# Kernel optimization log

Measured on AMD Instinct MI355X. Metric: run time of the kernel, lower is better.

## Reference

```python
import jax, jax.numpy as jnp
import numpy as np

B, C, N, T = 16, 32, 1024, 128
R = 10  # low-rank bottleneck of W1/W2


def setup_inputs() -> dict:
    key = jax.random.key(0)
    k1, k2, k3, k4 = jax.random.split(key, 4)
    x = jax.random.normal(k1, (B, C, N, T), dtype=jnp.float32)
    W1 = jax.random.normal(k2, (R, N), dtype=jnp.float32) * 0.05
    W2 = jax.random.normal(k3, (R, N), dtype=jnp.float32) * 0.05
    alpha = jax.random.normal(k4, (C,), dtype=jnp.float32) * 0.1
    return {"x": x, "W1": W1, "W2": W2, "alpha": alpha}


def reference(x, W1, W2, alpha):
    # k = q = einsum('bint,i->btn', x, alpha): contract channels -> [B, T, N]
    k = jnp.einsum('bcnt,c->btn', x, alpha)
    # low-rank bilinear scores: (k @ W1^T) @ (k @ W2^T)^T -> [B, T, T]
    kw1 = jnp.einsum('btn,rn->btr', k, W1)   # [B, T, R]
    qw2 = jnp.einsum('btn,rn->btr', k, W2)   # [B, T, R]
    scores = jnp.einsum('btr,bsr->bts', kw1, qw2)  # [B, T, T]
    att = jax.nn.softmax(scores, axis=-1)
    # weighted sum over time: einsum('bti,bcni->bcnt', att, x)
    return jnp.einsum('bts,bcns->bcnt', att, x)
```

## Files before the change

kernel.cpp:

```cpp
#include <hip/hip_runtime.h>
#include <hip/hip_bf16.h>


#define B_ 16
#define C_ 32
#define N_ 1024
#define T_ 128
#define R_ 10

typedef __bf16 bf16x8 __attribute__((ext_vector_type(8)));
typedef __bf16 bf16x4 __attribute__((ext_vector_type(4)));
typedef float f32x4 __attribute__((ext_vector_type(4)));

__global__ __launch_bounds__(256) void k_reduce_c(const float* __restrict__ x,
                                                  const float* __restrict__ alpha,
                                                  float* __restrict__ k) {
    int bid = blockIdx.x;
    int b   = bid >> 7;
    int nc  = bid & 127;
    int tid = threadIdx.x;
    int nl  = tid >> 5;
    int lc  = tid & 31;
    int n   = nc * 8 + nl;
    const float4* xb = reinterpret_cast<const float4*>(
        x + ((size_t)(b * C_) * N_ + n) * T_) + lc;
    float4 acc = {0.f, 0.f, 0.f, 0.f};
    #pragma unroll 8
    for (int c = 0; c < C_; ++c) {
        float a = alpha[c];
        float4 v = xb[(size_t)c * (N_ * T_ / 4)];
        acc.x += a * v.x; acc.y += a * v.y; acc.z += a * v.z; acc.w += a * v.w;
    }
    reinterpret_cast<float4*>(k + ((size_t)b * N_ + n) * T_)[lc] = acc;
}

__global__ __launch_bounds__(128) void kw_partial2(const float* __restrict__ k,
                                                   const float* __restrict__ W1,
                                                   const float* __restrict__ W2,
                                                   float* __restrict__ p1,
                                                   float* __restrict__ p2) {
    __shared__ float wl[32][20];
    int bid = blockIdx.x;
    int b   = bid >> 5;
    int ch  = bid & 31;
    int n0  = ch * 32;
    int t   = threadIdx.x;
    for (int i = t; i < 32 * 20; i += 128) {
        int nl = i & 31, q = i >> 5;
        wl[nl][q] = (q < 10) ? W1[q * N_ + n0 + nl] : W2[(q - 10) * N_ + n0 + nl];
    }
    __syncthreads();
    float a1[R_] = {}, a2[R_] = {};
    const float* kb = k + ((size_t)b * N_ + n0) * T_ + t;
    #pragma unroll 2
    for (int g = 0; g < 4; ++g) {
        float kv[8];
        #pragma unroll
        for (int j = 0; j < 8; ++j) kv[j] = kb[(g * 8 + j) * T_];
        #pragma unroll
        for (int j = 0; j < 8; ++j) {
            int nl = g * 8 + j;
            #pragma unroll
            for (int r = 0; r < R_; ++r) {
                a1[r] += kv[j] * wl[nl][r];
                a2[r] += kv[j] * wl[nl][10 + r];
            }
        }
    }
    #pragma unroll
    for (int r = 0; r < R_; ++r) {
        size_t o = (((size_t)b * R_ + r) * 32 + ch) * T_ + t;
        p1[o] = a1[r];
        p2[o] = a2[r];
    }
}

__global__ __launch_bounds__(128) void kw_reduce(const float* __restrict__ p1,
                                                 const float* __restrict__ p2,
                                                 float* __restrict__ kwc) {
    int bid = blockIdx.x;
    int b = bid / 20;
    int q = bid - b * 20;
    int w = q / 10;
    int r = q - w * 10;
    int t = threadIdx.x;
    const float* src = (w ? p2 : p1) + (((size_t)b * R_ + r) * 32) * T_ + t;
    float s = 0.f;
    #pragma unroll
    for (int ch = 0; ch < 32; ++ch) s += src[ch * T_];
    kwc[(((size_t)b * 2 + w) * R_ + r) * T_ + t] = s;
}

__global__ __launch_bounds__(128) void scores_softmax(const float* __restrict__ kwc,
                                                      __bf16* __restrict__ att) {
    __shared__ __align__(16) float kw1s[T_][12];
    __shared__ __align__(16) float kw2s[T_][12];
    __shared__ float sc[T_][T_ + 1];
    int b = blockIdx.x;
    int t = threadIdx.x;
    const float* kb = kwc + (size_t)b * 2 * R_ * T_;
    #pragma unroll
    for (int r = 0; r < R_; ++r) {
        kw1s[t][r] = kb[r * T_ + t];
        kw2s[t][r] = kb[(R_ + r) * T_ + t];
    }
    __syncthreads();
    float myw[R_];
    #pragma unroll
    for (int r = 0; r < R_; ++r) myw[r] = kw1s[t][r];
    float mx = -1e30f;
    for (int s = 0; s < T_; ++s) {
        float wv[12];
        const float4* qr = reinterpret_cast<const float4*>(&kw2s[s][0]);
        #pragma unroll
        for (int q = 0; q < 3; ++q) *reinterpret_cast<float4*>(&wv[q * 4]) = qr[q];
        float v = 0.f;
        #pragma unroll
        for (int r = 0; r < R_; ++r) v += myw[r] * wv[r];
        sc[t][s] = v;
        mx = fmaxf(mx, v);
    }
    float sum = 0.f;
    for (int s = 0; s < T_; ++s) {
        float e = __expf(sc[t][s] - mx);
        sc[t][s] = e;
        sum += e;
    }
    float inv = 1.0f / sum;
    __bf16* arow = att + ((size_t)b * T_ + t) * T_;
    for (int s8 = 0; s8 < T_; s8 += 8) {
        bf16x8 hv;
        #pragma unroll
        for (int q = 0; q < 8; ++q) hv[q] = (__bf16)(sc[t][s8 + q] * inv);
        *reinterpret_cast<bf16x8*>(arow + s8) = hv;
    }
}

__global__ __launch_bounds__(256, 4) void out_gemm2(const float* __restrict__ x,
                                                    const __bf16* __restrict__ att,
                                                    float* __restrict__ out) {
    __shared__ __align__(16) __bf16 attl[T_][T_];
    int bid = blockIdx.x;
    int nc  = bid & 15;
    int c   = (bid >> 4) & 31;
    int b   = bid >> 9;
    int tid = threadIdx.x;
    size_t slab = ((size_t)(b * C_ + c) * N_ + nc * 64) * T_;
    char* attb = (char*)&attl[0][0];

    const uint4* ga = reinterpret_cast<const uint4*>(att + (size_t)b * T_ * T_);
    #pragma unroll
    for (int i = 0; i < 8; ++i) {
        int e = i * 256 + tid, row = e >> 4;
        int bc = ((e & 15) * 16) ^ ((row & 7) << 4);
        *reinterpret_cast<uint4*>(attb + row * 256 + bc) = ga[e];
    }
    __syncthreads();

    int wave = tid >> 6, lane = tid & 63;
    int r16 = lane & 15, g = lane >> 4;
    int wt = wave & 1, wn = wave >> 1;
    int swz = (r16 & 7) << 4;

    const float* xr0 = x + slab + (size_t)(wn * 32 + r16) * T_ + g * 8;
    const float* xr1 = xr0 + 16 * T_;

    f32x4 acc[2][4] = {};
    float4 c0a = *reinterpret_cast<const float4*>(xr0);
    float4 c0b = *reinterpret_cast<const float4*>(xr0 + 4);
    float4 c1a = *reinterpret_cast<const float4*>(xr1);
    float4 c1b = *reinterpret_cast<const float4*>(xr1 + 4);
    #pragma unroll
    for (int ks = 0; ks < 4; ++ks) {
        float4 n0a, n0b, n1a, n1b;
        if (ks < 3) {
            int o = (ks + 1) * 32;
            n0a = *reinterpret_cast<const float4*>(xr0 + o);
            n0b = *reinterpret_cast<const float4*>(xr0 + o + 4);
            n1a = *reinterpret_cast<const float4*>(xr1 + o);
            n1b = *reinterpret_cast<const float4*>(xr1 + o + 4);
        }
        bf16x8 bx0 = {(__bf16)c0a.x, (__bf16)c0a.y, (__bf16)c0a.z, (__bf16)c0a.w,
                      (__bf16)c0b.x, (__bf16)c0b.y, (__bf16)c0b.z, (__bf16)c0b.w};
        bf16x8 bx1 = {(__bf16)c1a.x, (__bf16)c1a.y, (__bf16)c1a.z, (__bf16)c1a.w,
                      (__bf16)c1b.x, (__bf16)c1b.y, (__bf16)c1b.z, (__bf16)c1b.w};
        int kc = ks * 64 + g * 16;
        bf16x8 a[4];
        #pragma unroll
        for (int tt = 0; tt < 4; ++tt)
            a[tt] = *reinterpret_cast<const bf16x8*>(
                attb + (wt * 64 + tt * 16 + r16) * 256 + (kc ^ swz));
        #pragma unroll
        for (int tt = 0; tt < 4; ++tt)
            acc[0][tt] = __builtin_amdgcn_mfma_f32_16x16x32_bf16(a[tt], bx0, acc[0][tt], 0, 0, 0);
        #pragma unroll
        for (int tt = 0; tt < 4; ++tt)
            acc[1][tt] = __builtin_amdgcn_mfma_f32_16x16x32_bf16(a[tt], bx1, acc[1][tt], 0, 0, 0);
        c0a = n0a; c0b = n0b; c1a = n1a; c1b = n1b;
    }
    float* o = out + slab;
    #pragma unroll
    for (int nn = 0; nn < 2; ++nn) {
        int n_l = wn * 32 + nn * 16 + r16;
        #pragma unroll
        for (int tt = 0; tt < 4; ++tt)
            *reinterpret_cast<f32x4*>(o + (size_t)n_l * T_ + (wt * 64 + tt * 16 + g * 4)) = acc[nn][tt];
    }
}

extern "C" void kernel_launch(void* const* d_in, const int* in_sizes, int n_in,
                              void* d_out, int out_size, void* d_ws, size_t ws_size,
                              hipStream_t stream) {
    const float* x     = (const float*)d_in[0];
    const float* W1    = (const float*)d_in[1];
    const float* W2    = (const float*)d_in[2];
    const float* alpha = (const float*)d_in[3];
    float* out = (float*)d_out;

    float* k    = (float*)d_ws;
    float* p1   = k   + (size_t)B_ * N_ * T_;
    float* p2   = p1  + (size_t)B_ * R_ * 32 * T_;
    float* kwc  = p2  + (size_t)B_ * R_ * 32 * T_;
    __bf16* att = (__bf16*)(kwc + (size_t)B_ * 2 * R_ * T_);

    k_reduce_c   <<<dim3(B_ * (N_ / 8)), dim3(256), 0, stream>>>(x, alpha, k);
    kw_partial2  <<<dim3(B_ * 32),       dim3(128), 0, stream>>>(k, W1, W2, p1, p2);
    kw_reduce    <<<dim3(B_ * 20),       dim3(128), 0, stream>>>(p1, p2, kwc);
    scores_softmax<<<dim3(B_),           dim3(128), 0, stream>>>(kwc, att);
    out_gemm2    <<<dim3(B_ * 512),      dim3(256), 0, stream>>>(x, att, out);
}
```

Measured before the change: 214.3 us.

## Stage x tiles in LDS and loop four n-chunks per block, reusing att

```diff
diff --git a/kernel.cpp b/kernel.cpp
--- a/kernel.cpp
+++ b/kernel.cpp
@@ -136,24 +136,39 @@
     }
 }
 
-__global__ __launch_bounds__(256, 4) void out_gemm2(const float* __restrict__ x,
+__global__ __launch_bounds__(256, 3) void out_gemm3(const float* __restrict__ x,
                                                     const __bf16* __restrict__ att,
                                                     float* __restrict__ out) {
     __shared__ __align__(16) __bf16 attl[T_][T_];
-    int bid = blockIdx.x;
-    int nc  = bid & 15;
-    int c   = (bid >> 4) & 31;
-    int b   = bid >> 9;
+    __shared__ __align__(16) __bf16 xsl[64][T_];
+    int bid = blockIdx.x;
+    int sg  = bid & 3;
+    int c   = (bid >> 2) & 31;
+    int b   = bid >> 7;
     int tid = threadIdx.x;
-    size_t slab = ((size_t)(b * C_ + c) * N_ + nc * 64) * T_;
     char* attb = (char*)&attl[0][0];
+    char* xbb  = (char*)&xsl[0][0];
+    size_t slab0 = ((size_t)(b * C_ + c) * N_ + (sg * 4) * 64) * T_;
 
     const uint4* ga = reinterpret_cast<const uint4*>(att + (size_t)b * T_ * T_);
+    uint4 ar[8];
+    #pragma unroll
+    for (int i = 0; i < 8; ++i) ar[i] = ga[i * 256 + tid];
+    const float4* gx0 = reinterpret_cast<const float4*>(x + slab0);
+    float4 xr[8];
+    #pragma unroll
+    for (int j = 0; j < 8; ++j) xr[j] = gx0[j * 256 + tid];
     #pragma unroll
     for (int i = 0; i < 8; ++i) {
         int e = i * 256 + tid, row = e >> 4;
         int bc = ((e & 15) * 16) ^ ((row & 7) << 4);
-        *reinterpret_cast<uint4*>(attb + row * 256 + bc) = ga[e];
+        *reinterpret_cast<uint4*>(attb + row * 256 + bc) = ar[i];
+    }
+    #pragma unroll
+    for (int j = 0; j < 8; ++j) {
+        int e = j * 256 + tid, row = e >> 5;
+        bf16x4 hv = {(__bf16)xr[j].x, (__bf16)xr[j].y, (__bf16)xr[j].z, (__bf16)xr[j].w};
+        *reinterpret_cast<bf16x4*>(xbb + row * 256 + (((e & 31) * 8) ^ ((row & 7) << 4))) = hv;
     }
     __syncthreads();
 
@@ -162,49 +177,55 @@
     int wt = wave & 1, wn = wave >> 1;
     int swz = (r16 & 7) << 4;
 
-    const float* xr0 = x + slab + (size_t)(wn * 32 + r16) * T_ + g * 8;
-    const float* xr1 = xr0 + 16 * T_;
-
-    f32x4 acc[2][4] = {};
-    float4 c0a = *reinterpret_cast<const float4*>(xr0);
-    float4 c0b = *reinterpret_cast<const float4*>(xr0 + 4);
-    float4 c1a = *reinterpret_cast<const float4*>(xr1);
-    float4 c1b = *reinterpret_cast<const float4*>(xr1 + 4);
-    #pragma unroll
-    for (int ks = 0; ks < 4; ++ks) {
-        float4 n0a, n0b, n1a, n1b;
-        if (ks < 3) {
-            int o = (ks + 1) * 32;
-            n0a = *reinterpret_cast<const float4*>(xr0 + o);
-            n0b = *reinterpret_cast<const float4*>(xr0 + o + 4);
-            n1a = *reinterpret_cast<const float4*>(xr1 + o);
-            n1b = *reinterpret_cast<const float4*>(xr1 + o + 4);
-        }
-        bf16x8 bx0 = {(__bf16)c0a.x, (__bf16)c0a.y, (__bf16)c0a.z, (__bf16)c0a.w,
-                      (__bf16)c0b.x, (__bf16)c0b.y, (__bf16)c0b.z, (__bf16)c0b.w};
-        bf16x8 bx1 = {(__bf16)c1a.x, (__bf16)c1a.y, (__bf16)c1a.z, (__bf16)c1a.w,
-                      (__bf16)c1b.x, (__bf16)c1b.y, (__bf16)c1b.z, (__bf16)c1b.w};
-        int kc = ks * 64 + g * 16;
-        bf16x8 a[4];
-        #pragma unroll
-        for (int tt = 0; tt < 4; ++tt)
-            a[tt] = *reinterpret_cast<const bf16x8*>(
-                attb + (wt * 64 + tt * 16 + r16) * 256 + (kc ^ swz));
-        #pragma unroll
-        for (int tt = 0; tt < 4; ++tt)
-            acc[0][tt] = __builtin_amdgcn_mfma_f32_16x16x32_bf16(a[tt], bx0, acc[0][tt], 0, 0, 0);
-        #pragma unroll
-        for (int tt = 0; tt < 4; ++tt)
-            acc[1][tt] = __builtin_amdgcn_mfma_f32_16x16x32_bf16(a[tt], bx1, acc[1][tt], 0, 0, 0);
-        c0a = n0a; c0b = n0b; c1a = n1a; c1b = n1b;
-    }
-    float* o = out + slab;
-    #pragma unroll
-    for (int nn = 0; nn < 2; ++nn) {
-        int n_l = wn * 32 + nn * 16 + r16;
-        #pragma unroll
-        for (int tt = 0; tt < 4; ++tt)
-            *reinterpret_cast<f32x4*>(o + (size_t)n_l * T_ + (wt * 64 + tt * 16 + g * 4)) = acc[nn][tt];
+    for (int i = 0; i < 4; ++i) {
+        float4 xn[8];
+        if (i < 3) {
+            const float4* gxn = reinterpret_cast<const float4*>(
+                x + slab0 + ((size_t)(i + 1) * 64) * T_);
+            #pragma unroll
+            for (int j = 0; j < 8; ++j) xn[j] = gxn[j * 256 + tid];
+        }
+        f32x4 acc[2][4] = {};
+        #pragma unroll
+        for (int ks = 0; ks < 4; ++ks) {
+            int kc = ks * 64 + g * 16;
+            bf16x8 a[4], bx[2];
+            #pragma unroll
+            for (int tt = 0; tt < 4; ++tt)
+                a[tt] = *reinterpret_cast<const bf16x8*>(
+                    attb + (wt * 64 + tt * 16 + r16) * 256 + (kc ^ swz));
+            #pragma unroll
+            for (int nn = 0; nn < 2; ++nn)
+                bx[nn] = *reinterpret_cast<const bf16x8*>(
+                    xbb + (wn * 32 + nn * 16 + r16) * 256 + (kc ^ swz));
+            #pragma unroll
+            for (int nn = 0; nn < 2; ++nn)
+                #pragma unroll
+                for (int tt = 0; tt < 4; ++tt)
+                    acc[nn][tt] = __builtin_amdgcn_mfma_f32_16x16x32_bf16(
+                        a[tt], bx[nn], acc[nn][tt], 0, 0, 0);
+        }
+        float* o = out + slab0 + ((size_t)i * 64) * T_;
+        #pragma unroll
+        for (int nn = 0; nn < 2; ++nn) {
+            int n_l = wn * 32 + nn * 16 + r16;
+            #pragma unroll
+            for (int tt = 0; tt < 4; ++tt)
+                *reinterpret_cast<f32x4*>(
+                    o + (size_t)n_l * T_ + (wt * 64 + tt * 16 + g * 4)) = acc[nn][tt];
+        }
+        if (i < 3) {
+            __syncthreads();
+            #pragma unroll
+            for (int j = 0; j < 8; ++j) {
+                int e = j * 256 + tid, row = e >> 5;
+                bf16x4 hv = {(__bf16)xn[j].x, (__bf16)xn[j].y,
+                             (__bf16)xn[j].z, (__bf16)xn[j].w};
+                *reinterpret_cast<bf16x4*>(
+                    xbb + row * 256 + (((e & 31) * 8) ^ ((row & 7) << 4))) = hv;
+            }
+            __syncthreads();
+        }
     }
 }
 
@@ -227,5 +248,5 @@
     kw_partial2  <<<dim3(B_ * 32),       dim3(128), 0, stream>>>(k, W1, W2, p1, p2);
     kw_reduce    <<<dim3(B_ * 20),       dim3(128), 0, stream>>>(p1, p2, kwc);
     scores_softmax<<<dim3(B_),           dim3(128), 0, stream>>>(kwc, att);
-    out_gemm2    <<<dim3(B_ * 512),      dim3(256), 0, stream>>>(x, att, out);
-}
+    out_gemm3    <<<dim3(B_ * C_ * 4),   dim3(256), 0, stream>>>(x, att, out);
+}
```

Result: faster. 186.2 us (-13.1%).

## Make out GEMM blocks cover 256 rows with a register double-buffered x prefetch

Applied to the files above, without the earlier changes.

```diff
diff --git a/kernel.cpp b/kernel.cpp
--- a/kernel.cpp
+++ b/kernel.cpp
@@ -11,6 +11,12 @@
 typedef __bf16 bf16x8 __attribute__((ext_vector_type(8)));
 typedef __bf16 bf16x4 __attribute__((ext_vector_type(4)));
 typedef float f32x4 __attribute__((ext_vector_type(4)));
+
+__device__ __forceinline__ void lds_barrier() {
+    asm volatile("s_waitcnt lgkmcnt(0)" ::: "memory");
+    __builtin_amdgcn_s_barrier();
+    asm volatile("" ::: "memory");
+}
 
 __global__ __launch_bounds__(256) void k_reduce_c(const float* __restrict__ x,
                                                   const float* __restrict__ alpha,
@@ -136,76 +142,82 @@
     }
 }
 
-__global__ __launch_bounds__(256, 4) void out_gemm2(const float* __restrict__ x,
+#define SLAB_BODY(XCUR, XNXT, I)                                              \
+    {                                                                         \
+        bf16x8 bx[4];                                                         \
+        _Pragma("unroll")                                                     \
+        for (int ks = 0; ks < 4; ++ks) {                                      \
+            float4 lo = XCUR[2 * ks], hi = XCUR[2 * ks + 1];                  \
+            bx[ks] = (bf16x8){(__bf16)lo.x, (__bf16)lo.y, (__bf16)lo.z,       \
+                              (__bf16)lo.w, (__bf16)hi.x, (__bf16)hi.y,       \
+                              (__bf16)hi.z, (__bf16)hi.w};                    \
+        }                                                                     \
+        if ((I) < 3) {                                                        \
+            const float* xr = xrow + (size_t)((I) + 1) * 64 * T_;             \
+            _Pragma("unroll")                                                 \
+            for (int q = 0; q < 8; ++q)                                       \
+                XNXT[q] = *reinterpret_cast<const float4*>(                   \
+                    xr + (q >> 1) * 32 + (q & 1) * 4);                        \
+        }                                                                     \
+        f32x4 acc[8] = {};                                                    \
+        _Pragma("unroll")                                                     \
+        for (int ks = 0; ks < 4; ++ks) {                                      \
+            int kc = ks * 64 + g * 16;                                        \
+            bf16x8 a[8];                                                      \
+            _Pragma("unroll")                                                 \
+            for (int tt = 0; tt < 8; ++tt)                                    \
+                a[tt] = *reinterpret_cast<const bf16x8*>(                     \
+                    attb + (tt * 16 + r16) * 256 + (kc ^ swz));               \
+            _Pragma("unroll")                                                 \
+            for (int tt = 0; tt < 8; ++tt)                                    \
+                acc[tt] = __builtin_amdgcn_mfma_f32_16x16x32_bf16(            \
+                    a[tt], bx[ks], acc[tt], 0, 0, 0);                         \
+        }                                                                     \
+        float* o = out + slab0 + (size_t)((I) * 64 + wave * 16 + r16) * T_;   \
+        _Pragma("unroll")                                                     \
+        for (int tt = 0; tt < 8; ++tt)                                        \
+            *reinterpret_cast<f32x4*>(o + tt * 16 + g * 4) = acc[tt];         \
+    }
+
+__global__ __launch_bounds__(256, 3) void out_gemm5(const float* __restrict__ x,
                                                     const __bf16* __restrict__ att,
                                                     float* __restrict__ out) {
     __shared__ __align__(16) __bf16 attl[T_][T_];
     int bid = blockIdx.x;
-    int nc  = bid & 15;
-    int c   = (bid >> 4) & 31;
-    int b   = bid >> 9;
+    int sg  = bid & 3;
+    int c   = (bid >> 2) & 31;
+    int b   = bid >> 7;
     int tid = threadIdx.x;
-    size_t slab = ((size_t)(b * C_ + c) * N_ + nc * 64) * T_;
     char* attb = (char*)&attl[0][0];
+    size_t slab0 = ((size_t)(b * C_ + c) * N_ + sg * 256) * T_;
 
     const uint4* ga = reinterpret_cast<const uint4*>(att + (size_t)b * T_ * T_);
+    uint4 ar[8];
+    #pragma unroll
+    for (int i = 0; i < 8; ++i) ar[i] = ga[i * 256 + tid];
+
+    int wave = tid >> 6, lane = tid & 63;
+    int r16 = lane & 15, g = lane >> 4;
+    int swz = (r16 & 7) << 4;
+    const float* xrow = x + slab0 + (size_t)(wave * 16 + r16) * T_ + g * 8;
+
+    float4 xa[8], xb[8];
+    #pragma unroll
+    for (int q = 0; q < 8; ++q)
+        xa[q] = *reinterpret_cast<const float4*>(xrow + (q >> 1) * 32 + (q & 1) * 4);
+
     #pragma unroll
     for (int i = 0; i < 8; ++i) {
         int e = i * 256 + tid, row = e >> 4;
         int bc = ((e & 15) * 16) ^ ((row & 7) << 4);
-        *reinterpret_cast<uint4*>(attb + row * 256 + bc) = ga[e];
-    }
-    __syncthreads();
-
-    int wave = tid >> 6, lane = tid & 63;
-    int r16 = lane & 15, g = lane >> 4;
-    int wt = wave & 1, wn = wave >> 1;
-    int swz = (r16 & 7) << 4;
-
-    const float* xr0 = x + slab + (size_t)(wn * 32 + r16) * T_ + g * 8;
-    const float* xr1 = xr0 + 16 * T_;
-
-    f32x4 acc[2][4] = {};
-    float4 c0a = *reinterpret_cast<const float4*>(xr0);
-    float4 c0b = *reinterpret_cast<const float4*>(xr0 + 4);
-    float4 c1a = *reinterpret_cast<const float4*>(xr1);
-    float4 c1b = *reinterpret_cast<const float4*>(xr1 + 4);
-    #pragma unroll
-    for (int ks = 0; ks < 4; ++ks) {
-        float4 n0a, n0b, n1a, n1b;
-        if (ks < 3) {
-            int o = (ks + 1) * 32;
-            n0a = *reinterpret_cast<const float4*>(xr0 + o);
-            n0b = *reinterpret_cast<const float4*>(xr0 + o + 4);
-            n1a = *reinterpret_cast<const float4*>(xr1 + o);
-            n1b = *reinterpret_cast<const float4*>(xr1 + o + 4);
-        }
-        bf16x8 bx0 = {(__bf16)c0a.x, (__bf16)c0a.y, (__bf16)c0a.z, (__bf16)c0a.w,
-                      (__bf16)c0b.x, (__bf16)c0b.y, (__bf16)c0b.z, (__bf16)c0b.w};
-        bf16x8 bx1 = {(__bf16)c1a.x, (__bf16)c1a.y, (__bf16)c1a.z, (__bf16)c1a.w,
-                      (__bf16)c1b.x, (__bf16)c1b.y, (__bf16)c1b.z, (__bf16)c1b.w};
-        int kc = ks * 64 + g * 16;
-        bf16x8 a[4];
-        #pragma unroll
-        for (int tt = 0; tt < 4; ++tt)
-            a[tt] = *reinterpret_cast<const bf16x8*>(
-                attb + (wt * 64 + tt * 16 + r16) * 256 + (kc ^ swz));
-        #pragma unroll
-        for (int tt = 0; tt < 4; ++tt)
-            acc[0][tt] = __builtin_amdgcn_mfma_f32_16x16x32_bf16(a[tt], bx0, acc[0][tt], 0, 0, 0);
-        #pragma unroll
-        for (int tt = 0; tt < 4; ++tt)
-            acc[1][tt] = __builtin_amdgcn_mfma_f32_16x16x32_bf16(a[tt], bx1, acc[1][tt], 0, 0, 0);
-        c0a = n0a; c0b = n0b; c1a = n1a; c1b = n1b;
-    }
-    float* o = out + slab;
-    #pragma unroll
-    for (int nn = 0; nn < 2; ++nn) {
-        int n_l = wn * 32 + nn * 16 + r16;
-        #pragma unroll
-        for (int tt = 0; tt < 4; ++tt)
-            *reinterpret_cast<f32x4*>(o + (size_t)n_l * T_ + (wt * 64 + tt * 16 + g * 4)) = acc[nn][tt];
-    }
+        *reinterpret_cast<uint4*>(attb + row * 256 + bc) = ar[i];
+    }
+    lds_barrier();
+
+    SLAB_BODY(xa, xb, 0)
+    SLAB_BODY(xb, xa, 1)
+    SLAB_BODY(xa, xb, 2)
+    SLAB_BODY(xb, xa, 3)
 }
 
 extern "C" void kernel_launch(void* const* d_in, const int* in_sizes, int n_in,
@@ -227,5 +239,5 @@
     kw_partial2  <<<dim3(B_ * 32),       dim3(128), 0, stream>>>(k, W1, W2, p1, p2);
     kw_reduce    <<<dim3(B_ * 20),       dim3(128), 0, stream>>>(p1, p2, kwc);
     scores_softmax<<<dim3(B_),           dim3(128), 0, stream>>>(kwc, att);
-    out_gemm2    <<<dim3(B_ * 512),      dim3(256), 0, stream>>>(x, att, out);
-}
+    out_gemm5    <<<dim3(B_ * C_ * 4),   dim3(256), 0, stream>>>(x, att, out);
+}
```

Measured after the change: 197.5 us. 7.9% less time.

## Fuse kw reduction into softmax and read attention directly from global in GEMM

Applied to the files above, without the earlier changes.

```diff
diff --git a/kernel.cpp b/kernel.cpp
--- a/kernel.cpp
+++ b/kernel.cpp
@@ -9,7 +9,6 @@
 #define R_ 10
 
 typedef __bf16 bf16x8 __attribute__((ext_vector_type(8)));
-typedef __bf16 bf16x4 __attribute__((ext_vector_type(4)));
 typedef float f32x4 __attribute__((ext_vector_type(4)));
 
 __global__ __launch_bounds__(256) void k_reduce_c(const float* __restrict__ x,
@@ -75,34 +74,22 @@
     }
 }
 
-__global__ __launch_bounds__(128) void kw_reduce(const float* __restrict__ p1,
-                                                 const float* __restrict__ p2,
-                                                 float* __restrict__ kwc) {
-    int bid = blockIdx.x;
-    int b = bid / 20;
-    int q = bid - b * 20;
-    int w = q / 10;
-    int r = q - w * 10;
-    int t = threadIdx.x;
-    const float* src = (w ? p2 : p1) + (((size_t)b * R_ + r) * 32) * T_ + t;
-    float s = 0.f;
-    #pragma unroll
-    for (int ch = 0; ch < 32; ++ch) s += src[ch * T_];
-    kwc[(((size_t)b * 2 + w) * R_ + r) * T_ + t] = s;
-}
-
-__global__ __launch_bounds__(128) void scores_softmax(const float* __restrict__ kwc,
-                                                      __bf16* __restrict__ att) {
+__global__ __launch_bounds__(128) void scores_softmax3(const float* __restrict__ p1,
+                                                       const float* __restrict__ p2,
+                                                       __bf16* __restrict__ att) {
     __shared__ __align__(16) float kw1s[T_][12];
     __shared__ __align__(16) float kw2s[T_][12];
     __shared__ float sc[T_][T_ + 1];
     int b = blockIdx.x;
     int t = threadIdx.x;
-    const float* kb = kwc + (size_t)b * 2 * R_ * T_;
     #pragma unroll
     for (int r = 0; r < R_; ++r) {
-        kw1s[t][r] = kb[r * T_ + t];
-        kw2s[t][r] = kb[(R_ + r) * T_ + t];
+        float s1 = 0.f, s2 = 0.f;
+        const float* q1 = p1 + (((size_t)b * R_ + r) * 32) * T_ + t;
+        const float* q2 = p2 + (((size_t)b * R_ + r) * 32) * T_ + t;
+        #pragma unroll 4
+        for (int ch = 0; ch < 32; ++ch) { s1 += q1[ch * T_]; s2 += q2[ch * T_]; }
+        kw1s[t][r] = s1; kw2s[t][r] = s2;
     }
     __syncthreads();
     float myw[R_];
@@ -136,76 +123,45 @@
     }
 }
 
-__global__ __launch_bounds__(256, 4) void out_gemm2(const float* __restrict__ x,
+__global__ __launch_bounds__(256, 4) void out_gemm7(const float* __restrict__ x,
                                                     const __bf16* __restrict__ att,
                                                     float* __restrict__ out) {
-    __shared__ __align__(16) __bf16 attl[T_][T_];
     int bid = blockIdx.x;
-    int nc  = bid & 15;
+    int ng  = bid & 15;
     int c   = (bid >> 4) & 31;
     int b   = bid >> 9;
     int tid = threadIdx.x;
-    size_t slab = ((size_t)(b * C_ + c) * N_ + nc * 64) * T_;
-    char* attb = (char*)&attl[0][0];
-
-    const uint4* ga = reinterpret_cast<const uint4*>(att + (size_t)b * T_ * T_);
-    #pragma unroll
-    for (int i = 0; i < 8; ++i) {
-        int e = i * 256 + tid, row = e >> 4;
-        int bc = ((e & 15) * 16) ^ ((row & 7) << 4);
-        *reinterpret_cast<uint4*>(attb + row * 256 + bc) = ga[e];
-    }
-    __syncthreads();
-
     int wave = tid >> 6, lane = tid & 63;
     int r16 = lane & 15, g = lane >> 4;
-    int wt = wave & 1, wn = wave >> 1;
-    int swz = (r16 & 7) << 4;
+    int n = ng * 64 + wave * 16 + r16;
 
-    const float* xr0 = x + slab + (size_t)(wn * 32 + r16) * T_ + g * 8;
-    const float* xr1 = xr0 + 16 * T_;
+    const float* xr = x + ((size_t)(b * C_ + c) * N_ + n) * T_ + g * 8;
+    const char* ab  = (const char*)att + (size_t)b * (T_ * T_ * 2) +
+                      r16 * 256 + g * 16;
+    float* o = out + ((size_t)(b * C_ + c) * N_ + n) * T_ + g * 4;
 
-    f32x4 acc[2][4] = {};
-    float4 c0a = *reinterpret_cast<const float4*>(xr0);
-    float4 c0b = *reinterpret_cast<const float4*>(xr0 + 4);
-    float4 c1a = *reinterpret_cast<const float4*>(xr1);
-    float4 c1b = *reinterpret_cast<const float4*>(xr1 + 4);
+    float4 xf[8];
+    #pragma unroll
+    for (int q = 0; q < 8; ++q)
+        xf[q] = *reinterpret_cast<const float4*>(xr + (q >> 1) * 32 + (q & 1) * 4);
+
+    f32x4 acc[8] = {};
     #pragma unroll
     for (int ks = 0; ks < 4; ++ks) {
-        float4 n0a, n0b, n1a, n1b;
-        if (ks < 3) {
-            int o = (ks + 1) * 32;
-            n0a = *reinterpret_cast<const float4*>(xr0 + o);
-            n0b = *reinterpret_cast<const float4*>(xr0 + o + 4);
-            n1a = *reinterpret_cast<const float4*>(xr1 + o);
-            n1b = *reinterpret_cast<const float4*>(xr1 + o + 4);
-        }
-        bf16x8 bx0 = {(__bf16)c0a.x, (__bf16)c0a.y, (__bf16)c0a.z, (__bf16)c0a.w,
-                      (__bf16)c0b.x, (__bf16)c0b.y, (__bf16)c0b.z, (__bf16)c0b.w};
-        bf16x8 bx1 = {(__bf16)c1a.x, (__bf16)c1a.y, (__bf16)c1a.z, (__bf16)c1a.w,
-                      (__bf16)c1b.x, (__bf16)c1b.y, (__bf16)c1b.z, (__bf16)c1b.w};
-        int kc = ks * 64 + g * 16;
-        bf16x8 a[4];
+        float4 lo = xf[2 * ks], hi = xf[2 * ks + 1];
+        bf16x8 bx = {(__bf16)lo.x, (__bf16)lo.y, (__bf16)lo.z, (__bf16)lo.w,
+                     (__bf16)hi.x, (__bf16)hi.y, (__bf16)hi.z, (__bf16)hi.w};
+        bf16x8 a[8];
         #pragma unroll
-        for (int tt = 0; tt < 4; ++tt)
-            a[tt] = *reinterpret_cast<const bf16x8*>(
-                attb + (wt * 64 + tt * 16 + r16) * 256 + (kc ^ swz));
+        for (int tt = 0; tt < 8; ++tt)
+            a[tt] = *reinterpret_cast<const bf16x8*>(ab + tt * 4096 + ks * 64);
         #pragma unroll
-        for (int tt = 0; tt < 4; ++tt)
-            acc[0][tt] = __builtin_amdgcn_mfma_f32_16x16x32_bf16(a[tt], bx0, acc[0][tt], 0, 0, 0);
-        #pragma unroll
-        for (int tt = 0; tt < 4; ++tt)
-            acc[1][tt] = __builtin_amdgcn_mfma_f32_16x16x32_bf16(a[tt], bx1, acc[1][tt], 0, 0, 0);
-        c0a = n0a; c0b = n0b; c1a = n1a; c1b = n1b;
+        for (int tt = 0; tt < 8; ++tt)
+            acc[tt] = __builtin_amdgcn_mfma_f32_16x16x32_bf16(a[tt], bx, acc[tt], 0, 0, 0);
     }
-    float* o = out + slab;
     #pragma unroll
-    for (int nn = 0; nn < 2; ++nn) {
-        int n_l = wn * 32 + nn * 16 + r16;
-        #pragma unroll
-        for (int tt = 0; tt < 4; ++tt)
-            *reinterpret_cast<f32x4*>(o + (size_t)n_l * T_ + (wt * 64 + tt * 16 + g * 4)) = acc[nn][tt];
-    }
+    for (int tt = 0; tt < 8; ++tt)
+        *reinterpret_cast<f32x4*>(o + tt * 16) = acc[tt];
 }
 
 extern "C" void kernel_launch(void* const* d_in, const int* in_sizes, int n_in,
@@ -217,15 +173,15 @@
     const float* alpha = (const float*)d_in[3];
     float* out = (float*)d_out;
 
+    const size_t KSZ = (size_t)B_ * N_ * T_;
+    const size_t PSZ = (size_t)B_ * R_ * 32 * T_;
     float* k    = (float*)d_ws;
-    float* p1   = k   + (size_t)B_ * N_ * T_;
-    float* p2   = p1  + (size_t)B_ * R_ * 32 * T_;
-    float* kwc  = p2  + (size_t)B_ * R_ * 32 * T_;
-    __bf16* att = (__bf16*)(kwc + (size_t)B_ * 2 * R_ * T_);
+    float* p1   = k + KSZ;
+    float* p2   = p1 + PSZ;
+    __bf16* att = (__bf16*)(p2 + PSZ);
 
-    k_reduce_c   <<<dim3(B_ * (N_ / 8)), dim3(256), 0, stream>>>(x, alpha, k);
-    kw_partial2  <<<dim3(B_ * 32),       dim3(128), 0, stream>>>(k, W1, W2, p1, p2);
-    kw_reduce    <<<dim3(B_ * 20),       dim3(128), 0, stream>>>(p1, p2, kwc);
-    scores_softmax<<<dim3(B_),           dim3(128), 0, stream>>>(kwc, att);
-    out_gemm2    <<<dim3(B_ * 512),      dim3(256), 0, stream>>>(x, att, out);
+    k_reduce_c     <<<dim3(B_ * (N_ / 8)), dim3(256), 0, stream>>>(x, alpha, k);
+    kw_partial2    <<<dim3(B_ * 32),       dim3(128), 0, stream>>>(k, W1, W2, p1, p2);
+    scores_softmax3<<<dim3(B_),            dim3(128), 0, stream>>>(p1, p2, att);
+    out_gemm7      <<<dim3(B_ * C_ * 16),  dim3(256), 0, stream>>>(x, att, out);
 }
```

New measurement: 300.7 us. +40.3%, slower.
